# Performance work log

Measured on AMD Instinct MI355X. Metric: run time of the kernel, lower is better.

## Reference

```python
import jax, jax.numpy as jnp
import numpy as np

N_NODES = 50000   # batch_size * num_nodes
N_EDGES = 800000
D_IN = 128
D_OUT = 128


def setup_inputs() -> dict:
    key = jax.random.key(0)
    k1, k2, k3, k4 = jax.random.split(key, 4)
    x = jax.random.normal(k1, (N_NODES, D_IN), dtype=jnp.float32)
    edge_index = jax.random.randint(k2, (2, N_EDGES), 0, N_NODES, dtype=jnp.int64)
    W = jax.random.normal(k3, (D_OUT, D_IN), dtype=jnp.float32) * (1.0 / np.sqrt(D_IN))
    b = jax.random.normal(k4, (D_OUT,), dtype=jnp.float32) * 0.01
    return {"x": x, "edge_index": edge_index, "batch_size": 50, "num_nodes": 1000, "W": W, "b": b}


def reference(x, edge_index, batch_size, num_nodes, W, b):
    dim_size = batch_size * num_nodes
    row, col = edge_index[0], edge_index[1]
    # gather messages and segment-mean aggregate over destination rows
    msgs = x[col]                                   # [E, D_IN]
    summed = jax.ops.segment_sum(msgs, row, num_segments=dim_size)      # [N, D_IN]
    counts = jax.ops.segment_sum(jnp.ones((row.shape[0],), dtype=x.dtype), row,
                                 num_segments=dim_size)                 # [N]
    mean = summed / jnp.maximum(counts, 1.0)[:, None]                   # 0 for empty rows
    # linear projection (torch Linear: y = x @ W.T + b)
    return mean @ W.T + b
```

## Files before the change

kernel.cpp:

```cpp
#include <hip/hip_runtime.h>

#define D 128
#define BSHIFT 5
#define BCAP 1024
#define EPB_A 2048

typedef unsigned short ushort_t;
typedef unsigned int uint_t;
typedef __attribute__((ext_vector_type(8))) short short8_t;
typedef __attribute__((ext_vector_type(4))) float f32x4_t;
typedef __attribute__((ext_vector_type(4))) uint_t uint4_t;
typedef const __attribute__((address_space(1))) void* gas_cptr;
typedef __attribute__((address_space(3))) void* las_ptr;
typedef const __attribute__((address_space(3))) ushort_t* las_cushort;

__device__ __forceinline__ bool eidx_is64(const int* eidx) {
    int lane = threadIdx.x & 63;
    int probe = eidx[2 * lane + 1];
    return __ballot(probe != 0) == 0ULL;
}

__device__ __forceinline__ uint_t f2bf(float f) {
    union { float f; uint_t i; } v; v.f = f;
    return (v.i + 0x7fffu + ((v.i >> 16) & 1u)) >> 16;
}
__device__ __forceinline__ float bf_lo(uint_t w) {
    union { uint_t i; float f; } v; v.i = w << 16; return v.f;
}
__device__ __forceinline__ float bf_hi(uint_t w) {
    union { uint_t i; float f; } v; v.i = w & 0xffff0000u; return v.f;
}

__global__ __launch_bounds__(256) void pre_kernel(
    const int* __restrict__ eidx, int* __restrict__ gcur,
    int* __restrict__ bucket, int E, int NBUK, int ab,
    const float* __restrict__ x, uint_t* __restrict__ xb, int total8, int cvb,
    const float* __restrict__ Wsrc, uint_t* __restrict__ wb, int N) {
    int t = threadIdx.x;

    if ((int)blockIdx.x >= ab) {
        if (xb == nullptr) return;
        int cb = blockIdx.x - ab;
        if (cb < cvb) {
            int i = cb * 256 + t;
            if (i < total8) {
                const float4* p = (const float4*)(x + (size_t)i * 8);
                float4 a = p[0], b = p[1];
                uint4 o;
                o.x = f2bf(a.x) | (f2bf(a.y) << 16);
                o.y = f2bf(a.z) | (f2bf(a.w) << 16);
                o.z = f2bf(b.x) | (f2bf(b.y) << 16);
                o.w = f2bf(b.z) | (f2bf(b.w) << 16);
                *(uint4*)(xb + (size_t)i * 4) = o;
            }
            if (cb == 0 && t < 16) {
                uint4 z; z.x = 0u; z.y = 0u; z.z = 0u; z.w = 0u;
                ((uint4*)(xb + (size_t)N * (D / 2)))[t] = z;
            }
        } else {
            int i = (cb - cvb) * 256 + t;
            if (i < D * D / 8) {
                const float4* p = (const float4*)(Wsrc + (size_t)i * 8);
                float4 a = p[0], b = p[1];
                uint4 o;
                o.x = f2bf(a.x) | (f2bf(a.y) << 16);
                o.y = f2bf(a.z) | (f2bf(a.w) << 16);
                o.z = f2bf(b.x) | (f2bf(b.y) << 16);
                o.w = f2bf(b.z) | (f2bf(b.w) << 16);
                *(uint4*)(wb + (size_t)i * 4) = o;
            }
        }
        return;
    }

    __shared__ int lhist[2048];
    __shared__ int lbase[2048];
    bool is64 = eidx_is64(eidx);
    for (int i = t; i < NBUK; i += 256) lhist[i] = 0;
    __syncthreads();

    int e0 = blockIdx.x * EPB_A;
    int e1 = min(e0 + EPB_A, E);
    int base = e0 + 8 * t;
    int rr[8], cc[8];
    #pragma unroll
    for (int k = 0; k < 8; ++k) rr[k] = -1;
    if (is64) {
        if (base + 8 <= e1 && (E & 1) == 0) {
            const int4* rp = (const int4*)(eidx + 2 * (size_t)base);
            const int4* cp = (const int4*)(eidx + 2 * (size_t)E + 2 * (size_t)base);
            #pragma unroll
            for (int g = 0; g < 4; ++g) {
                int4 r = rp[g], c = cp[g];
                rr[2 * g]     = r.x; cc[2 * g]     = c.x;
                rr[2 * g + 1] = r.z; cc[2 * g + 1] = c.z;
            }
        } else {
            #pragma unroll
            for (int k = 0; k < 8; ++k) {
                int e = base + k;
                if (e < e1) { rr[k] = eidx[2 * e]; cc[k] = eidx[2 * E + 2 * e]; }
            }
        }
    } else {
        if (base + 8 <= e1 && (E & 3) == 0) {
            const int4* rp = (const int4*)(eidx + base);
            const int4* cp = (const int4*)(eidx + (size_t)E + base);
            int4 r0 = rp[0], r1 = rp[1], c0 = cp[0], c1 = cp[1];
            rr[0] = r0.x; rr[1] = r0.y; rr[2] = r0.z; rr[3] = r0.w;
            rr[4] = r1.x; rr[5] = r1.y; rr[6] = r1.z; rr[7] = r1.w;
            cc[0] = c0.x; cc[1] = c0.y; cc[2] = c0.z; cc[3] = c0.w;
            cc[4] = c1.x; cc[5] = c1.y; cc[6] = c1.z; cc[7] = c1.w;
        } else {
            #pragma unroll
            for (int k = 0; k < 8; ++k) {
                int e = base + k;
                if (e < e1) { rr[k] = eidx[e]; cc[k] = eidx[E + e]; }
            }
        }
    }
    #pragma unroll
    for (int k = 0; k < 8; ++k)
        if (rr[k] >= 0) atomicAdd(&lhist[rr[k] >> BSHIFT], 1);
    __syncthreads();
    for (int i = t; i < NBUK; i += 256) {
        int h = lhist[i];
        lbase[i] = (h > 0) ? atomicAdd(&gcur[i], h) : 0;
        lhist[i] = 0;
    }
    __syncthreads();
    #pragma unroll
    for (int k = 0; k < 8; ++k) {
        if (rr[k] >= 0) {
            int b = rr[k] >> BSHIFT;
            int p = atomicAdd(&lhist[b], 1);
            int idx = lbase[b] + p;
            if (idx < BCAP) bucket[b * BCAP + idx] = ((rr[k] & 31) << 24) | cc[k];
        }
    }
}

#define ISSUE(c, bufsel)                                                      \
    {                                                                         \
        ushort_t* db_ = wstage + (bufsel) * 2048;                             \
        __builtin_amdgcn_global_load_lds(                                     \
            (gas_cptr)(xb + (size_t)(c).x * D + 8 * sl),                      \
            (las_ptr)(db_), 16, 0, 0);                                        \
        __builtin_amdgcn_global_load_lds(                                     \
            (gas_cptr)(xb + (size_t)(c).y * D + 8 * sl),                      \
            (las_ptr)(db_ + 512), 16, 0, 0);                                  \
        __builtin_amdgcn_global_load_lds(                                     \
            (gas_cptr)(xb + (size_t)(c).z * D + 8 * sl),                      \
            (las_ptr)(db_ + 1024), 16, 0, 0);                                 \
        __builtin_amdgcn_global_load_lds(                                     \
            (gas_cptr)(xb + (size_t)(c).w * D + 8 * sl),                      \
            (las_ptr)(db_ + 1536), 16, 0, 0);                                 \
    }

#define ACCV(v)                                                               \
    a0 += bf_lo((v)[0]); a1 += bf_hi((v)[0]);                                 \
    a2 += bf_lo((v)[1]); a3 += bf_hi((v)[1]);                                 \
    a4 += bf_lo((v)[2]); a5 += bf_hi((v)[2]);                                 \
    a6 += bf_lo((v)[3]); a7 += bf_hi((v)[3]);

#define CONSUME                                                               \
    {                                                                         \
        uint4_t v0, v1, v2, v3;                                               \
        asm volatile("ds_read_b128 %0, %1"             : "=v"(v0) : "v"(sbp));\
        asm volatile("ds_read_b128 %0, %1 offset:1024" : "=v"(v1) : "v"(sbp));\
        asm volatile("ds_read_b128 %0, %1 offset:2048" : "=v"(v2) : "v"(sbp));\
        asm volatile("ds_read_b128 %0, %1 offset:3072" : "=v"(v3) : "v"(sbp));\
        asm volatile("s_waitcnt lgkmcnt(0)" ::: "memory");                    \
        __builtin_amdgcn_sched_barrier(0);                                    \
        ACCV(v0) ACCV(v1) ACCV(v2) ACCV(v3)                                   \
    }

__global__ __launch_bounds__(256, 2) void fused_bf_kernel(
    const ushort_t* __restrict__ xb, const int* __restrict__ gcur,
    const int* __restrict__ bucket, const ushort_t* __restrict__ Wb,
    const float* __restrict__ bias, float* __restrict__ out, int N) {
    __shared__ alignas(16) int sE[1152];
    __shared__ int lcnt[32], lpos[32], lstart[32];
    __shared__ alignas(16) ushort_t sA[32 * 136];
    __shared__ alignas(16) ushort_t stage[24576];
    int t = threadIdx.x;
    int b = blockIdx.x;

    if (t < 32) { lcnt[t] = 0; lpos[t] = 0; }
    __syncthreads();
    int tot = min(gcur[b], BCAP);
    const int* bp = bucket + (size_t)b * BCAP;
    int4 ev = make_int4(-1, -1, -1, -1);
    if (4 * t + 3 < tot) {
        ev = *(const int4*)(bp + 4 * t);
    } else {
        if (4 * t + 0 < tot) ev.x = bp[4 * t + 0];
        if (4 * t + 1 < tot) ev.y = bp[4 * t + 1];
        if (4 * t + 2 < tot) ev.z = bp[4 * t + 2];
        if (4 * t + 3 < tot) ev.w = bp[4 * t + 3];
    }
    if (ev.x >= 0) atomicAdd(&lcnt[ev.x >> 24], 1);
    if (ev.y >= 0) atomicAdd(&lcnt[ev.y >> 24], 1);
    if (ev.z >= 0) atomicAdd(&lcnt[ev.z >> 24], 1);
    if (ev.w >= 0) atomicAdd(&lcnt[ev.w >> 24], 1);
    __syncthreads();
    if (t == 0) {
        int run = 0;
        #pragma unroll
        for (int i = 0; i < 32; ++i) {
            lstart[i] = run;
            run += (lcnt[i] + 3) & ~3;
        }
    }
    __syncthreads();
    {
        int v[4] = { ev.x, ev.y, ev.z, ev.w };
        #pragma unroll
        for (int q = 0; q < 4; ++q) {
            if (v[q] >= 0) {
                int rl = v[q] >> 24;
                int p = atomicAdd(&lpos[rl], 1);
                int idx = lstart[rl] + p;
                if (idx < 1152) sE[idx] = v[q] & 0xFFFFFF;
            }
        }
    }
    if (t < 32) {
        int c0 = lcnt[t];
        int pe = (c0 + 3) & ~3;
        for (int p = c0; p < pe; ++p) {
            int idx = lstart[t] + p;
            if (idx < 1152) sE[idx] = N;
        }
    }
    __syncthreads();

    int lane = t & 63, wave = t >> 6;
    int qi = t >> 4, sl = t & 15;
    int nbase = b << BSHIFT;
    ushort_t* wstage = stage + wave * 6144;

    #pragma unroll
    for (int quad = 0; quad < 2; ++quad) {
        int n = 2 * qi + quad;
        int nr = lcnt[n];
        int st = lstart[n];
        int trips = ((nr + 3) & ~3) >> 2;
        int wmax = trips;
        wmax = max(wmax, __shfl_xor(wmax, 16));
        wmax = max(wmax, __shfl_xor(wmax, 32));
        float a0 = 0.f, a1 = 0.f, a2 = 0.f, a3 = 0.f;
        float a4 = 0.f, a5 = 0.f, a6 = 0.f, a7 = 0.f;
        if (wmax > 0) {
            int4 cc0 = (0 < trips) ? *(const int4*)(sE + st)
                                   : make_int4(N, N, N, N);
            ISSUE(cc0, 0)
            if (wmax > 1) {
                int4 cc1 = (1 < trips) ? *(const int4*)(sE + st + 4)
                                       : make_int4(N, N, N, N);
                ISSUE(cc1, 1)
            }
            __builtin_amdgcn_sched_barrier(0);
            int bsel = 0;
            for (int bt = 0; bt < wmax; ++bt) {
                if (bt + 2 < wmax) {
                    int nb = bsel + 2; if (nb >= 3) nb -= 3;
                    int4 cn = (bt + 2 < trips)
                        ? *(const int4*)(sE + st + 4 * (bt + 2))
                        : make_int4(N, N, N, N);
                    ISSUE(cn, nb)
                    __builtin_amdgcn_sched_barrier(0);
                    asm volatile("s_waitcnt vmcnt(8)" ::: "memory");
                } else if (bt + 1 < wmax) {
                    asm volatile("s_waitcnt vmcnt(4)" ::: "memory");
                } else {
                    asm volatile("s_waitcnt vmcnt(0)" ::: "memory");
                }
                __builtin_amdgcn_sched_barrier(0);
                las_cushort sbp = (las_cushort)(wstage + bsel * 2048 + lane * 8);
                CONSUME
                bsel = (bsel == 2) ? 0 : bsel + 1;
            }
        }
        float inv = (nr > 0) ? 1.0f / (float)nr : 0.0f;
        uint4 pk;
        pk.x = f2bf(a0 * inv) | (f2bf(a1 * inv) << 16);
        pk.y = f2bf(a2 * inv) | (f2bf(a3 * inv) << 16);
        pk.z = f2bf(a4 * inv) | (f2bf(a5 * inv) << 16);
        pk.w = f2bf(a6 * inv) | (f2bf(a7 * inv) << 16);
        *(uint4*)(sA + n * 136 + 8 * sl) = pk;
    }
    __syncthreads();

    {
        int rt = wave & 1, jgrp = wave >> 1;
        int ml = lane & 15, kh = lane >> 4;
        short8_t afr[4];
        #pragma unroll
        for (int ks = 0; ks < 4; ++ks)
            afr[ks] = *(const short8_t*)(sA + (rt * 16 + ml) * 136 + ks * 32 + kh * 8);
        f32x4_t acc[4];
        #pragma unroll
        for (int q = 0; q < 4; ++q) acc[q] = (f32x4_t){0.f, 0.f, 0.f, 0.f};
        #pragma unroll
        for (int q = 0; q < 4; ++q) {
            int j = (jgrp * 4 + q) * 16 + ml;
            #pragma unroll
            for (int ks = 0; ks < 4; ++ks) {
                short8_t bfr = *(const short8_t*)(Wb + (size_t)j * D + ks * 32 + kh * 8);
                acc[q] = __builtin_amdgcn_mfma_f32_16x16x32_bf16(afr[ks], bfr, acc[q], 0, 0, 0);
            }
        }
        #pragma unroll
        for (int q = 0; q < 4; ++q) {
            int j = (jgrp * 4 + q) * 16 + ml;
            float bj = bias[j];
            #pragma unroll
            for (int r = 0; r < 4; ++r) {
                int gn = nbase + rt * 16 + kh * 4 + r;
                if (gn < N) out[(size_t)gn * D + j] = acc[q][r] + bj;
            }
        }
    }
}

__global__ __launch_bounds__(256) void prep_kernel(
    const int* __restrict__ gcur, const int* __restrict__ bucket,
    int* __restrict__ elist, int* __restrict__ cnt,
    int* __restrict__ start, int N, int NBUK) {
    __shared__ int lcnt[32], lpos[32], lstart[32];
    int t = threadIdx.x;
    int b = blockIdx.x;
    if (t < 32) { lcnt[t] = 0; lpos[t] = 0; }
    __syncthreads();
    int tot = min(gcur[b], BCAP);
    const int* bp = bucket + (size_t)b * BCAP;
    for (int i = t; i < tot; i += 256)
        atomicAdd(&lcnt[bp[i] >> 24], 1);
    __syncthreads();
    if (t == 0) {
        int run = 0;
        #pragma unroll
        for (int i = 0; i < 32; ++i) {
            lstart[i] = run;
            run += (lcnt[i] + 3) & ~3;
        }
    }
    __syncthreads();
    for (int i = t; i < tot; i += 256) {
        int v = bp[i];
        int rl = v >> 24;
        int p = atomicAdd(&lpos[rl], 1);
        int idx = lstart[rl] + p;
        if (idx < BCAP) elist[(size_t)b * BCAP + idx] = v & 0xFFFFFF;
    }
    if (t < 32) {
        int gr = (b << BSHIFT) + t;
        if (gr < N) { cnt[gr] = lcnt[t]; start[gr] = b * BCAP + lstart[t]; }
    }
}

__global__ __launch_bounds__(256, 6) void fused_kernel(
    const float* __restrict__ x, const int* __restrict__ elist,
    const int* __restrict__ cnt, const int* __restrict__ start,
    const float* __restrict__ W, const float* __restrict__ bias,
    float* __restrict__ out, int N) {
    __shared__ float sT[128 * 36];
    __shared__ float wc[16 * 132];
    int t = threadIdx.x;
    int lane = t & 63, wave = t >> 6;
    int half = lane >> 5, sl = lane & 31;
    int nbase = blockIdx.x * 32;

    #pragma unroll
    for (int pair = 0; pair < 4; ++pair) {
        int n = wave * 8 + pair * 2 + half;
        int gn = nbase + n;
        int nr  = (gn < N) ? cnt[gn]   : 0;
        int beg = (gn < N) ? start[gn] : 0;
        int nro  = __shfl(nr, lane ^ 32);
        int both = min(nr, nro);
        float ax = 0.f, ay = 0.f, az = 0.f, aw = 0.f;
        int i = 0;
        for (; i + 8 <= both; i += 8) {
            int4 cA = *(const int4*)(elist + beg + i);
            int4 cB = *(const int4*)(elist + beg + i + 4);
            float4 v0 = *(const float4*)(x + (size_t)cA.x * D + 4 * sl);
            float4 v1 = *(const float4*)(x + (size_t)cA.y * D + 4 * sl);
            float4 v2 = *(const float4*)(x + (size_t)cA.z * D + 4 * sl);
            float4 v3 = *(const float4*)(x + (size_t)cA.w * D + 4 * sl);
            float4 v4 = *(const float4*)(x + (size_t)cB.x * D + 4 * sl);
            float4 v5 = *(const float4*)(x + (size_t)cB.y * D + 4 * sl);
            float4 v6 = *(const float4*)(x + (size_t)cB.z * D + 4 * sl);
            float4 v7 = *(const float4*)(x + (size_t)cB.w * D + 4 * sl);
            ax += ((v0.x + v1.x) + (v2.x + v3.x)) + ((v4.x + v5.x) + (v6.x + v7.x));
            ay += ((v0.y + v1.y) + (v2.y + v3.y)) + ((v4.y + v5.y) + (v6.y + v7.y));
            az += ((v0.z + v1.z) + (v2.z + v3.z)) + ((v4.z + v5.z) + (v6.z + v7.z));
            aw += ((v0.w + v1.w) + (v2.w + v3.w)) + ((v4.w + v5.w) + (v6.w + v7.w));
        }
        for (; i < nr; ++i) {
            int c0 = elist[beg + i];
            float4 v = *(const float4*)(x + (size_t)c0 * D + 4 * sl);
            ax += v.x; ay += v.y; az += v.z; aw += v.w;
        }
        float inv = (nr > 0) ? 1.0f / (float)nr : 0.0f;
        int k0 = 4 * sl;
        sT[(k0 + 0) * 36 + n] = ax * inv;
        sT[(k0 + 1) * 36 + n] = ay * inv;
        sT[(k0 + 2) * 36 + n] = az * inv;
        sT[(k0 + 3) * 36 + n] = aw * inv;
    }

    int jg = t & 31, ng = t >> 5;
    int j0 = jg * 4, n0 = ng * 4;
    float acc[4][4] = {};
    for (int kc = 0; kc < 8; ++kc) {
        __syncthreads();
        #pragma unroll
        for (int i = 0; i < 8; ++i) {
            int idx = t + i * 256;
            int j = idx >> 4, kk = idx & 15;
            wc[kk * 132 + j] = W[j * D + kc * 16 + kk];
        }
        __syncthreads();
        #pragma unroll
        for (int kk = 0; kk < 16; ++kk) {
            int k = kc * 16 + kk;
            float4 s4 = *(const float4*)(sT + k * 36 + n0);
            float4 w4 = *(const float4*)(wc + kk * 132 + j0);
            acc[0][0] = fmaf(s4.x, w4.x, acc[0][0]); acc[0][1] = fmaf(s4.x, w4.y, acc[0][1]);
            acc[0][2] = fmaf(s4.x, w4.z, acc[0][2]); acc[0][3] = fmaf(s4.x, w4.w, acc[0][3]);
            acc[1][0] = fmaf(s4.y, w4.x, acc[1][0]); acc[1][1] = fmaf(s4.y, w4.y, acc[1][1]);
            acc[1][2] = fmaf(s4.y, w4.z, acc[1][2]); acc[1][3] = fmaf(s4.y, w4.w, acc[1][3]);
            acc[2][0] = fmaf(s4.z, w4.x, acc[2][0]); acc[2][1] = fmaf(s4.z, w4.y, acc[2][1]);
            acc[2][2] = fmaf(s4.z, w4.z, acc[2][2]); acc[2][3] = fmaf(s4.z, w4.w, acc[2][3]);
            acc[3][0] = fmaf(s4.w, w4.x, acc[3][0]); acc[3][1] = fmaf(s4.w, w4.y, acc[3][1]);
            acc[3][2] = fmaf(s4.w, w4.z, acc[3][2]); acc[3][3] = fmaf(s4.w, w4.w, acc[3][3]);
        }
    }
    float4 b4 = *(const float4*)(bias + j0);
    #pragma unroll
    for (int i = 0; i < 4; ++i) {
        int gn = nbase + n0 + i;
        if (gn >= N) continue;
        float4 o;
        o.x = acc[i][0] + b4.x;
        o.y = acc[i][1] + b4.y;
        o.z = acc[i][2] + b4.z;
        o.w = acc[i][3] + b4.w;
        *(float4*)(out + (size_t)gn * D + j0) = o;
    }
}

__global__ __launch_bounds__(256) void scatter_kernel(
    const float* __restrict__ x, const int* __restrict__ eidx,
    float* summed, float* __restrict__ counts, int E) {
    int t = blockIdx.x * 256 + threadIdx.x;
    int lane = threadIdx.x & 63;
    bool is64 = eidx_is64(eidx);
    int e = t >> 6;
    if (e >= E) return;
    int d = lane * 2;
    int r, c;
    if (is64) { r = eidx[2 * e]; c = eidx[2 * E + 2 * e]; }
    else      { r = eidx[e];     c = eidx[E + e]; }
    float2 v = *(const float2*)(x + (size_t)c * D + d);
    float* dst = summed + (size_t)r * D + d;
    atomicAdd(dst, v.x);
    atomicAdd(dst + 1, v.y);
    if (lane == 0) atomicAdd(counts + r, 1.0f);
}

__global__ __launch_bounds__(256) void divide_kernel(
    float* __restrict__ sums, const float* __restrict__ counts, int N) {
    int g = blockIdx.x * 256 + threadIdx.x;
    int r = g >> 6, lane = g & 63;
    if (r >= N) return;
    float inv = 1.0f / fmaxf(counts[r], 1.0f);
    float2* p = (float2*)(sums + (size_t)r * D + 2 * lane);
    float2 v = *p;
    v.x *= inv; v.y *= inv;
    *p = v;
}

__global__ __launch_bounds__(256) void gemm_kernel(
    float* inout, const float* __restrict__ W,
    const float* __restrict__ bias, int N) {
    __shared__ float sT[128 * 36];
    __shared__ float wc[32 * 132];
    int t = threadIdx.x;
    int nbase = blockIdx.x * 32;
    #pragma unroll
    for (int i = 0; i < 16; ++i) {
        int idx = t + i * 256;
        int n = idx >> 7, k = idx & 127;
        int gn = nbase + n;
        sT[k * 36 + n] = (gn < N) ? inout[(size_t)gn * D + k] : 0.0f;
    }
    int jg = t & 31, ng = t >> 5;
    int j0 = jg * 4, n0 = ng * 4;
    float acc[4][4] = {};
    for (int kc = 0; kc < 4; ++kc) {
        __syncthreads();
        #pragma unroll
        for (int i = 0; i < 16; ++i) {
            int idx = t + i * 256;
            int j = idx >> 5, kk = idx & 31;
            wc[kk * 132 + j] = W[j * D + kc * 32 + kk];
        }
        __syncthreads();
        #pragma unroll 8
        for (int kk = 0; kk < 32; ++kk) {
            int k = kc * 32 + kk;
            float4 s4 = *(const float4*)(sT + k * 36 + n0);
            float4 w4 = *(const float4*)(wc + kk * 132 + j0);
            acc[0][0] = fmaf(s4.x, w4.x, acc[0][0]); acc[0][1] = fmaf(s4.x, w4.y, acc[0][1]);
            acc[0][2] = fmaf(s4.x, w4.z, acc[0][2]); acc[0][3] = fmaf(s4.x, w4.w, acc[0][3]);
            acc[1][0] = fmaf(s4.y, w4.x, acc[1][0]); acc[1][1] = fmaf(s4.y, w4.y, acc[1][1]);
            acc[1][2] = fmaf(s4.y, w4.z, acc[1][2]); acc[1][3] = fmaf(s4.y, w4.w, acc[1][3]);
            acc[2][0] = fmaf(s4.z, w4.x, acc[2][0]); acc[2][1] = fmaf(s4.z, w4.y, acc[2][1]);
            acc[2][2] = fmaf(s4.z, w4.z, acc[2][2]); acc[2][3] = fmaf(s4.z, w4.w, acc[2][3]);
            acc[3][0] = fmaf(s4.w, w4.x, acc[3][0]); acc[3][1] = fmaf(s4.w, w4.y, acc[3][1]);
            acc[3][2] = fmaf(s4.w, w4.z, acc[3][2]); acc[3][3] = fmaf(s4.w, w4.w, acc[3][3]);
        }
    }
    float4 b4 = *(const float4*)(bias + j0);
    #pragma unroll
    for (int i = 0; i < 4; ++i) {
        int gn = nbase + n0 + i;
        if (gn >= N) continue;
        float4 o;
        o.x = acc[i][0] + b4.x;
        o.y = acc[i][1] + b4.y;
        o.z = acc[i][2] + b4.z;
        o.w = acc[i][3] + b4.w;
        *(float4*)(inout + (size_t)gn * D + j0) = o;
    }
}

extern "C" void kernel_launch(void* const* d_in, const int* in_sizes, int n_in,
                              void* d_out, int out_size, void* d_ws, size_t ws_size,
                              hipStream_t stream) {
    const float* x = (const float*)d_in[0];
    const int* eidx = (const int*)d_in[1];
    const float* W = (const float*)d_in[4];
    const float* b = (const float*)d_in[5];
    float* out = (float*)d_out;

    int N = in_sizes[0] / D;
    int E = in_sizes[1] / 2;
    int NBUK = (N + 31) >> BSHIFT;
    int ab = (E + EPB_A - 1) / EPB_A;

    size_t o0 = 0;
    size_t o_gc = o0;  o0 += ((size_t)NBUK * 4 + 255) & ~255ULL;
    size_t o_cn = o0;  o0 += ((size_t)N * 4 + 255) & ~255ULL;
    size_t o_st = o0;  o0 += ((size_t)N * 4 + 255) & ~255ULL;
    size_t o_bk = o0;  o0 += (size_t)NBUK * BCAP * 4;
    size_t o_el = o0;  o0 += (size_t)NBUK * BCAP * 4;
    size_t base_need = o0;
    size_t o_xb = o0;  o0 += (((size_t)(N + 1) * D * 2) + 255) & ~255ULL;
    size_t o_wb = o0;  size_t bf_need = o0 + (size_t)D * D * 2;

    bool cap_ok = (N <= 65536) && ((size_t)NBUK * BCAP >= (size_t)E);

    int cvb = (N * D / 8 + 255) / 256;
    int wvb = (D * D / 8 + 255) / 256;

    if (cap_ok && ws_size >= bf_need) {
        char* ws = (char*)d_ws;
        int*      gcur  = (int*)(ws + o_gc);
        int*      bkt   = (int*)(ws + o_bk);
        ushort_t* xb    = (ushort_t*)(ws + o_xb);
        ushort_t* wb    = (ushort_t*)(ws + o_wb);

        hipMemsetAsync(gcur, 0, (size_t)NBUK * 4, stream);
        pre_kernel<<<ab + cvb + wvb, 256, 0, stream>>>(
            eidx, gcur, bkt, E, NBUK, ab,
            x, (uint_t*)xb, N * D / 8, cvb, W, (uint_t*)wb, N);
        fused_bf_kernel<<<NBUK, 256, 0, stream>>>(xb, gcur, bkt, wb, b, out, N);
    } else if (cap_ok && ws_size >= base_need) {
        char* ws = (char*)d_ws;
        int* gcur  = (int*)(ws + o_gc);
        int* cnt   = (int*)(ws + o_cn);
        int* start = (int*)(ws + o_st);
        int* bkt   = (int*)(ws + o_bk);
        int* elist = (int*)(ws + o_el);
        int fb = (N + 31) / 32;

        hipMemsetAsync(gcur, 0, (size_t)NBUK * 4, stream);
        pre_kernel<<<ab, 256, 0, stream>>>(
            eidx, gcur, bkt, E, NBUK, ab,
            nullptr, nullptr, 0, 0, nullptr, nullptr, N);
        prep_kernel<<<NBUK, 256, 0, stream>>>(gcur, bkt, elist, cnt, start, N, NBUK);
        fused_kernel<<<fb, 256, 0, stream>>>(x, elist, cnt, start, W, b, out, N);
    } else {
        float* counts = (float*)d_ws;
        int fb = (N + 31) / 32;
        hipMemsetAsync(d_out, 0, (size_t)N * D * sizeof(float), stream);
        hipMemsetAsync(d_ws, 0, (size_t)N * sizeof(float), stream);
        int sb = (E * 64 + 255) / 256;
        scatter_kernel<<<sb, 256, 0, stream>>>(x, eidx, out, counts, E);
        int db = (N * 64 + 255) / 256;
        divide_kernel<<<db, 256, 0, stream>>>(out, counts, N);
        gemm_kernel<<<fb, 256, 0, stream>>>(out, W, b, N);
    }
}
```

Measured before the change: 161.0 us.

## Sort edges by source-node quartile and use double-buffered staging for higher occupancy

Within each destination row, edges are now sub-bucketed into four source-index quartiles so that gathers of x rows hit nearby addresses, which may improve cache locality. The per-wave LDS staging drops from triple to double buffering, and launch bounds are raised to three blocks per SM, cutting shared memory per block so more waves can be resident. The trade-off is a shallower prefetch pipeline (one batch in flight instead of two) and a slightly more expensive LDS counting phase with 128 counters.

```diff
diff --git a/kernel.cpp b/kernel.cpp
--- a/kernel.cpp
+++ b/kernel.cpp
@@ -175,18 +175,20 @@
         ACCV(v0) ACCV(v1) ACCV(v2) ACCV(v3)                                   \
     }
 
-__global__ __launch_bounds__(256, 2) void fused_bf_kernel(
+__global__ __launch_bounds__(256, 3) void fused_bf_kernel(
     const ushort_t* __restrict__ xb, const int* __restrict__ gcur,
     const int* __restrict__ bucket, const ushort_t* __restrict__ Wb,
     const float* __restrict__ bias, float* __restrict__ out, int N) {
     __shared__ alignas(16) int sE[1152];
-    __shared__ int lcnt[32], lpos[32], lstart[32];
+    __shared__ int lcnt4[128], lpos4[128], lstart4[128];
+    __shared__ int lcnt[32], lstart[32];
     __shared__ alignas(16) ushort_t sA[32 * 136];
-    __shared__ alignas(16) ushort_t stage[24576];
+    __shared__ alignas(16) ushort_t stage[16384];
     int t = threadIdx.x;
     int b = blockIdx.x;
-
-    if (t < 32) { lcnt[t] = 0; lpos[t] = 0; }
+    int h1 = N >> 2, h2 = N >> 1, h3 = (N >> 1) + (N >> 2);
+
+    if (t < 128) { lcnt4[t] = 0; lpos4[t] = 0; }
     __syncthreads();
     int tot = min(gcur[b], BCAP);
     const int* bp = bucket + (size_t)b * BCAP;
@@ -199,17 +201,31 @@
         if (4 * t + 2 < tot) ev.z = bp[4 * t + 2];
         if (4 * t + 3 < tot) ev.w = bp[4 * t + 3];
     }
-    if (ev.x >= 0) atomicAdd(&lcnt[ev.x >> 24], 1);
-    if (ev.y >= 0) atomicAdd(&lcnt[ev.y >> 24], 1);
-    if (ev.z >= 0) atomicAdd(&lcnt[ev.z >> 24], 1);
-    if (ev.w >= 0) atomicAdd(&lcnt[ev.w >> 24], 1);
+    {
+        int v[4] = { ev.x, ev.y, ev.z, ev.w };
+        #pragma unroll
+        for (int q = 0; q < 4; ++q) {
+            if (v[q] >= 0) {
+                int c  = v[q] & 0xFFFFFF;
+                int cq = (c >= h2) ? ((c >= h3) ? 3 : 2) : ((c >= h1) ? 1 : 0);
+                atomicAdd(&lcnt4[((v[q] >> 24) << 2) | cq], 1);
+            }
+        }
+    }
     __syncthreads();
     if (t == 0) {
         int run = 0;
         #pragma unroll
-        for (int i = 0; i < 32; ++i) {
-            lstart[i] = run;
-            run += (lcnt[i] + 3) & ~3;
+        for (int r = 0; r < 32; ++r) {
+            lstart[r] = run;
+            #pragma unroll
+            for (int q = 0; q < 4; ++q) {
+                lstart4[(r << 2) | q] = run;
+                run += lcnt4[(r << 2) | q];
+            }
+            int cr = run - lstart[r];
+            lcnt[r] = cr;
+            run += (-cr) & 3;
         }
     }
     __syncthreads();
@@ -218,10 +234,12 @@
         #pragma unroll
         for (int q = 0; q < 4; ++q) {
             if (v[q] >= 0) {
-                int rl = v[q] >> 24;
-                int p = atomicAdd(&lpos[rl], 1);
-                int idx = lstart[rl] + p;
-                if (idx < 1152) sE[idx] = v[q] & 0xFFFFFF;
+                int c  = v[q] & 0xFFFFFF;
+                int cq = (c >= h2) ? ((c >= h3) ? 3 : 2) : ((c >= h1) ? 1 : 0);
+                int slot = ((v[q] >> 24) << 2) | cq;
+                int p = atomicAdd(&lpos4[slot], 1);
+                int idx = lstart4[slot] + p;
+                if (idx < 1152) sE[idx] = c;
             }
         }
     }
@@ -238,7 +256,7 @@
     int lane = t & 63, wave = t >> 6;
     int qi = t >> 4, sl = t & 15;
     int nbase = b << BSHIFT;
-    ushort_t* wstage = stage + wave * 6144;
+    ushort_t* wstage = stage + (wave << 12);
 
     #pragma unroll
     for (int quad = 0; quad < 2; ++quad) {
@@ -255,31 +273,22 @@
             int4 cc0 = (0 < trips) ? *(const int4*)(sE + st)
                                    : make_int4(N, N, N, N);
             ISSUE(cc0, 0)
-            if (wmax > 1) {
-                int4 cc1 = (1 < trips) ? *(const int4*)(sE + st + 4)
-                                       : make_int4(N, N, N, N);
-                ISSUE(cc1, 1)
-            }
             __builtin_amdgcn_sched_barrier(0);
-            int bsel = 0;
             for (int bt = 0; bt < wmax; ++bt) {
-                if (bt + 2 < wmax) {
-                    int nb = bsel + 2; if (nb >= 3) nb -= 3;
-                    int4 cn = (bt + 2 < trips)
-                        ? *(const int4*)(sE + st + 4 * (bt + 2))
+                int buf = bt & 1;
+                if (bt + 1 < wmax) {
+                    int4 cn = (bt + 1 < trips)
+                        ? *(const int4*)(sE + st + 4 * (bt + 1))
                         : make_int4(N, N, N, N);
-                    ISSUE(cn, nb)
+                    ISSUE(cn, buf ^ 1)
                     __builtin_amdgcn_sched_barrier(0);
-                    asm volatile("s_waitcnt vmcnt(8)" ::: "memory");
-                } else if (bt + 1 < wmax) {
                     asm volatile("s_waitcnt vmcnt(4)" ::: "memory");
                 } else {
                     asm volatile("s_waitcnt vmcnt(0)" ::: "memory");
                 }
                 __builtin_amdgcn_sched_barrier(0);
-                las_cushort sbp = (las_cushort)(wstage + bsel * 2048 + lane * 8);
+                las_cushort sbp = (las_cushort)(wstage + buf * 2048 + lane * 8);
                 CONSUME
-                bsel = (bsel == 2) ? 0 : bsel + 1;
             }
         }
         float inv = (nr > 0) ? 1.0f / (float)nr : 0.0f;
```

Result: no change. 161.0 us (-0.0%).
